# Performance work log

Hardware: AMD Instinct MI355X
Metric: run time of the kernel (lower is better)

The kernel has to match this reference:

```python
import jax, jax.numpy as jnp
import numpy as np

HIDDEN = 6      # tiny MLP width
GRID_R = 16     # CAM grid resolution
NUM_LAYERS = 2  # num hidden layers == shared_cam.num_layers
OUT_DIM = 3
N_POINTS = 2_097_152
LN_EPS = 1e-5


def _bilinear_border(grid, xy):
    """F.grid_sample(mode='bilinear', padding_mode='border', align_corners=True)
    for point queries. grid: [C, R, R]; xy: [N, 2] in [-1, 1] with xy[:,0]=x
    (width) and xy[:,1]=y (height). Returns [N, C]."""
    R = grid.shape[-1]
    # align_corners=True mapping to pixel coords, border padding = clamp
    coords = jnp.clip((xy + 1.0) * 0.5 * (R - 1), 0.0, float(R - 1))
    ix, iy = coords[:, 0], coords[:, 1]
    x0f, y0f = jnp.floor(ix), jnp.floor(iy)
    wx, wy = ix - x0f, iy - y0f                       # [N]
    x0 = x0f.astype(jnp.int32)
    y0 = y0f.astype(jnp.int32)
    x1 = jnp.minimum(x0 + 1, R - 1)
    y1 = jnp.minimum(y0 + 1, R - 1)
    g00 = grid[:, y0, x0]  # [C, N]
    g01 = grid[:, y0, x1]
    g10 = grid[:, y1, x0]
    g11 = grid[:, y1, x1]
    top = g00 * (1.0 - wx) + g01 * wx
    bot = g10 * (1.0 - wx) + g11 * wx
    return (top * (1.0 - wy) + bot * wy).T            # [N, C]


def _layernorm(h, w, b):
    mu = jnp.mean(h, axis=-1, keepdims=True)
    var = jnp.mean((h - mu) ** 2, axis=-1, keepdims=True)  # biased, like torch LN
    return (h - mu) * jax.lax.rsqrt(var + LN_EPS) * w + b


def setup_inputs() -> dict:
    key = jax.random.key(0)
    ks = jax.random.split(key, 10)
    xy = jax.random.uniform(ks[0], (N_POINTS, 2), dtype=jnp.float32,
                            minval=-1.0, maxval=1.0)
    # CAM grids (init is ones/zeros; perturb so the math is exercised)
    gamma = 1.0 + 0.1 * jax.random.normal(ks[1], (NUM_LAYERS, HIDDEN, GRID_R, GRID_R), jnp.float32)
    beta = 0.1 * jax.random.normal(ks[2], (NUM_LAYERS, HIDDEN, GRID_R, GRID_R), jnp.float32)
    # Tiny MLP weights (Kaiming-ish scale)
    w_in = jax.random.normal(ks[3], (HIDDEN, 2), jnp.float32) / np.sqrt(2.0)
    b_in = 0.1 * jax.random.normal(ks[4], (HIDDEN,), jnp.float32)
    w_h = jax.random.normal(ks[5], (NUM_LAYERS - 1, HIDDEN, HIDDEN), jnp.float32) / np.sqrt(HIDDEN)
    b_h = 0.1 * jax.random.normal(ks[6], (NUM_LAYERS - 1, HIDDEN), jnp.float32)
    w_out = jax.random.normal(ks[7], (OUT_DIM, HIDDEN), jnp.float32) / np.sqrt(HIDDEN)
    b_out = 0.1 * jax.random.normal(ks[8], (OUT_DIM,), jnp.float32)
    ln_w = 1.0 + 0.05 * jax.random.normal(ks[9], (NUM_LAYERS, HIDDEN), jnp.float32)
    ln_b = jnp.zeros((NUM_LAYERS, HIDDEN), jnp.float32)
    return {"xy": xy, "gamma": gamma, "beta": beta, "w_in": w_in, "b_in": b_in,
            "w_h": w_h, "b_h": b_h, "w_out": w_out, "b_out": b_out,
            "ln_w": ln_w, "ln_b": ln_b}


def reference(xy, gamma, beta, w_in, b_in, w_h, b_h, w_out, b_out, ln_w, ln_b):
    # h = act(in_layer(xy))
    h = jax.nn.silu(xy @ w_in.T + b_in)                    # [N, HIDDEN]
    for i in range(NUM_LAYERS):
        if i > 0:
            h = jax.nn.silu(h @ w_h[i - 1].T + b_h[i - 1])
        g = _bilinear_border(gamma[i], xy)                 # [N, HIDDEN]
        bb = _bilinear_border(beta[i], xy)                 # [N, HIDDEN]
        h = g * _layernorm(h, ln_w[i], ln_b[i]) + bb
    return h @ w_out.T + b_out                             # [N, OUT_DIM]
```

## Files before the change

### kernel.cpp

```cpp
#include <hip/hip_runtime.h>
#include <hip/hip_fp16.h>
#include <stdint.h>

#define NPTS 2097152
#define BLOCK 256
#define PPT 4
#define NBLK (NPTS / (BLOCK * PPT))

typedef float f32x2 __attribute__((ext_vector_type(2)));

static __device__ __forceinline__ float rfl(float v) {
    return __int_as_float(__builtin_amdgcn_readfirstlane(__float_as_int(v)));
}
static __device__ __forceinline__ __half2 u2h(uint32_t u) {
    union { uint32_t i; __half2 h; } v; v.i = u; return v.h;
}
static __device__ __forceinline__ uint32_t h2u(__half2 h) {
    union { __half2 h; uint32_t i; } v; v.h = h; return v.i;
}
static __device__ __forceinline__ f32x2 fma2(f32x2 a, f32x2 b, f32x2 c) {
    return __builtin_elementwise_fma(a, b, c);
}
static __device__ __forceinline__ f32x2 silu2(f32x2 v) {
    f32x2 t = v * (-1.4426950408889634f);
    f32x2 e = { __builtin_amdgcn_exp2f(t.x), __builtin_amdgcn_exp2f(t.y) };
    f32x2 d = e + 1.0f;
    f32x2 r = { __builtin_amdgcn_rcpf(d.x), __builtin_amdgcn_rcpf(d.y) };
    return v * r;
}
static __device__ __forceinline__ void ln2_apply(f32x2* h, const f32x2* g, const f32x2* b)
{
    f32x2 mu = (h[0] + h[1] + h[2] + h[3] + h[4] + h[5]) * (1.0f / 6.0f);
    f32x2 d[6];
    f32x2 var = (f32x2)0.0f;
#pragma unroll
    for (int j = 0; j < 6; ++j) { d[j] = h[j] - mu; var = fma2(d[j], d[j], var); }
    f32x2 vv = var * (1.0f / 6.0f) + 1e-5f;
    f32x2 rs = { __builtin_amdgcn_rsqf(vv.x), __builtin_amdgcn_rsqf(vv.y) };
#pragma unroll
    for (int j = 0; j < 6; ++j)
        h[j] = fma2(g[j], d[j] * rs, b[j]);
}

__global__ __launch_bounds__(256) void pack_kernel(
    const float* __restrict__ gamma,
    const float* __restrict__ beta,
    const float* __restrict__ ln_w,
    const float* __restrict__ ln_b,
    uint32_t* __restrict__ ws)
{
    int idx = blockIdx.x * 256 + threadIdx.x;
    if (idx >= 3072) return;
    int l = (idx >= 1536) ? 1 : 0;
    int r = idx - l * 1536;
    int s = r >> 8;
    int cell = r & 255;
    int x = cell & 15;
    int x1 = (x < 15) ? x + 1 : 15;
    int rowb = cell - x;
    int ch0 = (s < 3) ? 2 * s : 2 * (s - 3);
    const float* gsrc = gamma + l * 1536 + ch0 * 256;
    float ga_lo = gsrc[rowb + x];
    float ga_hi = gsrc[256 + rowb + x];
    float gb_lo = gsrc[rowb + x1];
    float gb_hi = gsrc[256 + rowb + x1];
    float a_lo, a_hi, b_lo, b_hi;
    if (s < 3) {
        float w_lo = ln_w[6 * l + ch0];
        float w_hi = ln_w[6 * l + ch0 + 1];
        a_lo = ga_lo * w_lo; a_hi = ga_hi * w_hi;
        b_lo = gb_lo * w_lo; b_hi = gb_hi * w_hi;
    } else {
        const float* bsrc = beta + l * 1536 + ch0 * 256;
        float nb_lo = ln_b[6 * l + ch0];
        float nb_hi = ln_b[6 * l + ch0 + 1];
        a_lo = fmaf(ga_lo, nb_lo, bsrc[rowb + x]);
        a_hi = fmaf(ga_hi, nb_hi, bsrc[256 + rowb + x]);
        b_lo = fmaf(gb_lo, nb_lo, bsrc[rowb + x1]);
        b_hi = fmaf(gb_hi, nb_hi, bsrc[256 + rowb + x1]);
    }
    uint32_t* dst = ws + (l * 256 + cell) * 12 + 2 * s;
    dst[0] = h2u(__floats2half2_rn(a_lo, a_hi));
    dst[1] = h2u(__floats2half2_rn(b_lo, b_hi));
}

static __device__ __forceinline__ void interp6_c(
    const uint4* u,
    __half2 W00, __half2 W01, __half2 W10, __half2 W11,
    f32x2* g, f32x2* b, int c)
{
    uint32_t A[6]  = { u[0].x, u[0].z, u[1].x, u[1].z, u[2].x, u[2].z };
    uint32_t Bv[6] = { u[0].y, u[0].w, u[1].y, u[1].w, u[2].y, u[2].w };
    uint32_t C[6]  = { u[3].x, u[3].z, u[4].x, u[4].z, u[5].x, u[5].z };
    uint32_t D[6]  = { u[3].y, u[3].w, u[4].y, u[4].w, u[5].y, u[5].w };
#pragma unroll
    for (int s = 0; s < 6; ++s) {
        __half2 acc = __hmul2(u2h(A[s]), W00);
        acc = __hfma2(u2h(Bv[s]), W01, acc);
        acc = __hfma2(u2h(C[s]), W10, acc);
        acc = __hfma2(u2h(D[s]), W11, acc);
        float2 r = __half22float2(acc);
        if (s < 3) { g[2 * s][c] = r.x; g[2 * s + 1][c] = r.y; }
        else       { b[2 * (s - 3)][c] = r.x; b[2 * (s - 3) + 1][c] = r.y; }
    }
}

__global__ __launch_bounds__(BLOCK, 4) void camfield_kernel(
    const float* __restrict__ xy,
    const uint32_t* __restrict__ packed,
    const float* __restrict__ w_in,
    const float* __restrict__ b_in,
    const float* __restrict__ w_h,
    const float* __restrict__ b_h,
    const float* __restrict__ w_out,
    const float* __restrict__ b_out,
    float* __restrict__ out)
{
    __shared__ __align__(16) uint32_t sg[2][256][12];

    const int tid = threadIdx.x;

    const int p0 = (blockIdx.x * BLOCK + tid) * PPT;
    const float4* xv = (const float4*)(xy + 2 * p0);
    float4 q0 = xv[0];
    float4 q1 = xv[1];

    {
        const uint4* src = (const uint4*)packed;
        uint4* dst = (uint4*)&sg[0][0][0];
#pragma unroll
        for (int i = 0; i < 6; ++i)
            dst[tid + 256 * i] = src[tid + 256 * i];
    }

    float Win0[6], Win1[6], Bin[6], Wh[6][6], Bh[6], Wo[3][6], Bo[3];
#pragma unroll
    for (int j = 0; j < 6; ++j) {
        Win0[j] = w_in[2 * j];
        Win1[j] = w_in[2 * j + 1];
        Bin[j]  = b_in[j];
        Bh[j]   = rfl(b_h[j]);
#pragma unroll
        for (int k = 0; k < 6; ++k) Wh[j][k] = rfl(w_h[6 * j + k]);
    }
#pragma unroll
    for (int j = 0; j < 3; ++j) {
        Bo[j] = rfl(b_out[j]);
#pragma unroll
        for (int k = 0; k < 6; ++k) Wo[j][k] = rfl(w_out[6 * j + k]);
    }

    __syncthreads();

    float xs[4] = { q0.x, q0.z, q1.x, q1.z };
    float ys[4] = { q0.y, q0.w, q1.y, q1.w };

    float o[12];

#pragma unroll
    for (int pp = 0; pp < 2; ++pp) {
        __half2 Wq[2][4];
        const uint4* c4[2];
        f32x2 X, Y;
#pragma unroll
        for (int c = 0; c < 2; ++c) {
            const int p = 2 * pp + c;
            const float x = xs[p];
            const float y = ys[p];
            X[c] = x; Y[c] = y;
            float fx = fminf(fmaxf(fmaf(x, 7.5f, 7.5f), 0.0f), 15.0f);
            float fy = fminf(fmaxf(fmaf(y, 7.5f, 7.5f), 0.0f), 15.0f);
            int x0 = (int)fx; if (x0 > 14) x0 = 14;
            int y0 = (int)fy; if (y0 > 14) y0 = 14;
            float wx = fx - (float)x0;
            float wy = fy - (float)y0;
            float w11f = wx * wy;
            float w10f = wy - w11f;
            float w01f = wx - w11f;
            float w00f = 1.0f - wx - wy + w11f;
            Wq[c][0] = __float2half2_rn(w00f);
            Wq[c][1] = __float2half2_rn(w01f);
            Wq[c][2] = __float2half2_rn(w10f);
            Wq[c][3] = __float2half2_rn(w11f);
            c4[c] = (const uint4*)&sg[0][(y0 << 4) + x0][0];
        }

        uint4 u[2][6];
#pragma unroll
        for (int c = 0; c < 2; ++c) {
            u[c][0] = c4[c][0];  u[c][1] = c4[c][1];  u[c][2] = c4[c][2];
            u[c][3] = c4[c][48]; u[c][4] = c4[c][49]; u[c][5] = c4[c][50];
        }

        f32x2 h2[6];
#pragma unroll
        for (int j = 0; j < 6; ++j)
            h2[j] = silu2(fma2(X, (f32x2)Win0[j], fma2(Y, (f32x2)Win1[j], (f32x2)Bin[j])));

        f32x2 G[6], Bb[6];
        interp6_c(u[0], Wq[0][0], Wq[0][1], Wq[0][2], Wq[0][3], G, Bb, 0);
        interp6_c(u[1], Wq[1][0], Wq[1][1], Wq[1][2], Wq[1][3], G, Bb, 1);
        ln2_apply(h2, G, Bb);

        uint4 v[2][6];
#pragma unroll
        for (int c = 0; c < 2; ++c) {
            v[c][0] = c4[c][768]; v[c][1] = c4[c][769]; v[c][2] = c4[c][770];
            v[c][3] = c4[c][816]; v[c][4] = c4[c][817]; v[c][5] = c4[c][818];
        }

        f32x2 t2[6];
#pragma unroll
        for (int j = 0; j < 6; ++j) {
            f32x2 a = (f32x2)Bh[j];
#pragma unroll
            for (int k = 0; k < 6; ++k) a = fma2(h2[k], (f32x2)Wh[j][k], a);
            t2[j] = silu2(a);
        }

        interp6_c(v[0], Wq[0][0], Wq[0][1], Wq[0][2], Wq[0][3], G, Bb, 0);
        interp6_c(v[1], Wq[1][0], Wq[1][1], Wq[1][2], Wq[1][3], G, Bb, 1);
        ln2_apply(t2, G, Bb);

#pragma unroll
        for (int j = 0; j < 3; ++j) {
            f32x2 a = (f32x2)Bo[j];
#pragma unroll
            for (int k = 0; k < 6; ++k) a = fma2(t2[k], (f32x2)Wo[j][k], a);
            o[3 * (2 * pp) + j]     = a.x;
            o[3 * (2 * pp + 1) + j] = a.y;
        }
    }

    float4* op = (float4*)(out + 3 * p0);
#pragma unroll
    for (int q = 0; q < 3; ++q)
        op[q] = make_float4(o[4 * q], o[4 * q + 1], o[4 * q + 2], o[4 * q + 3]);
}

extern "C" void kernel_launch(void* const* d_in, const int* in_sizes, int n_in,
                              void* d_out, int out_size, void* d_ws, size_t ws_size,
                              hipStream_t stream) {
    pack_kernel<<<12, 256, 0, stream>>>(
        (const float*)d_in[1],
        (const float*)d_in[2],
        (const float*)d_in[9],
        (const float*)d_in[10],
        (uint32_t*)d_ws);
    camfield_kernel<<<NBLK, BLOCK, 0, stream>>>(
        (const float*)d_in[0],
        (const uint32_t*)d_ws,
        (const float*)d_in[3],
        (const float*)d_in[4],
        (const float*)d_in[5],
        (const float*)d_in[6],
        (const float*)d_in[7],
        (const float*)d_in[8],
        (float*)d_out);
}
```

Baseline: 103.1 us.

## Interleave LDS grid gathers with LayerNorm stats and shrink register footprint

Restructures the per-pair loop so the bilinear gathers are issued row by row per point and interleaved with the LayerNorm mean/variance computation, instead of loading all twelve uint4 per point up front. This lowers live registers and overlaps LDS latency with ALU work. It also merges the two SiLU reciprocals into one shared rcp, makes w_in wave-uniform via readfirstlane, and writes outputs per iteration rather than buffering all twelve. The shared reciprocal changes rounding slightly and can overflow for large intermediate values.

```diff
diff --git a/kernel.cpp b/kernel.cpp
--- a/kernel.cpp
+++ b/kernel.cpp
@@ -25,21 +25,18 @@
     f32x2 t = v * (-1.4426950408889634f);
     f32x2 e = { __builtin_amdgcn_exp2f(t.x), __builtin_amdgcn_exp2f(t.y) };
     f32x2 d = e + 1.0f;
-    f32x2 r = { __builtin_amdgcn_rcpf(d.x), __builtin_amdgcn_rcpf(d.y) };
-    return v * r;
-}
-static __device__ __forceinline__ void ln2_apply(f32x2* h, const f32x2* g, const f32x2* b)
-{
+    float r = __builtin_amdgcn_rcpf(d.x * d.y);
+    f32x2 inv = { r * d.y, r * d.x };
+    return v * inv;
+}
+static __device__ __forceinline__ void ln2_prep(const f32x2* h, f32x2* d, f32x2* rs) {
     f32x2 mu = (h[0] + h[1] + h[2] + h[3] + h[4] + h[5]) * (1.0f / 6.0f);
-    f32x2 d[6];
     f32x2 var = (f32x2)0.0f;
 #pragma unroll
     for (int j = 0; j < 6; ++j) { d[j] = h[j] - mu; var = fma2(d[j], d[j], var); }
     f32x2 vv = var * (1.0f / 6.0f) + 1e-5f;
-    f32x2 rs = { __builtin_amdgcn_rsqf(vv.x), __builtin_amdgcn_rsqf(vv.y) };
-#pragma unroll
-    for (int j = 0; j < 6; ++j)
-        h[j] = fma2(g[j], d[j] * rs, b[j]);
+    f32x2 r = { __builtin_amdgcn_rsqf(vv.x), __builtin_amdgcn_rsqf(vv.y) };
+    *rs = r;
 }
 
 __global__ __launch_bounds__(256) void pack_kernel(
@@ -84,25 +81,48 @@
     dst[1] = h2u(__floats2half2_rn(b_lo, b_hi));
 }
 
-static __device__ __forceinline__ void interp6_c(
-    const uint4* u,
-    __half2 W00, __half2 W01, __half2 W10, __half2 W11,
-    f32x2* g, f32x2* b, int c)
-{
-    uint32_t A[6]  = { u[0].x, u[0].z, u[1].x, u[1].z, u[2].x, u[2].z };
-    uint32_t Bv[6] = { u[0].y, u[0].w, u[1].y, u[1].w, u[2].y, u[2].w };
-    uint32_t C[6]  = { u[3].x, u[3].z, u[4].x, u[4].z, u[5].x, u[5].z };
-    uint32_t D[6]  = { u[3].y, u[3].w, u[4].y, u[4].w, u[5].y, u[5].w };
+static __device__ __forceinline__ void interp_row(
+    uint4 r0, uint4 r1, uint4 r2, __half2 Wa, __half2 Wb, __half2* acc, bool first)
+{
+    uint32_t A[6] = { r0.x, r0.z, r1.x, r1.z, r2.x, r2.z };
+    uint32_t B[6] = { r0.y, r0.w, r1.y, r1.w, r2.y, r2.w };
 #pragma unroll
     for (int s = 0; s < 6; ++s) {
-        __half2 acc = __hmul2(u2h(A[s]), W00);
-        acc = __hfma2(u2h(Bv[s]), W01, acc);
-        acc = __hfma2(u2h(C[s]), W10, acc);
-        acc = __hfma2(u2h(D[s]), W11, acc);
-        float2 r = __half22float2(acc);
-        if (s < 3) { g[2 * s][c] = r.x; g[2 * s + 1][c] = r.y; }
-        else       { b[2 * (s - 3)][c] = r.x; b[2 * (s - 3) + 1][c] = r.y; }
-    }
+        __half2 t = first ? __hmul2(u2h(A[s]), Wa) : __hfma2(u2h(A[s]), Wa, acc[s]);
+        acc[s] = __hfma2(u2h(B[s]), Wb, t);
+    }
+}
+
+static __device__ __forceinline__ void interp_point(
+    const uint4* base, int off, const __half2* W, f32x2* G, f32x2* Bb, int c)
+{
+    uint4 r0 = base[off], r1 = base[off + 1], r2 = base[off + 2];
+    __half2 acc[6];
+    interp_row(r0, r1, r2, W[0], W[1], acc, true);
+    uint4 s0 = base[off + 48], s1 = base[off + 49], s2 = base[off + 50];
+    interp_row(s0, s1, s2, W[2], W[3], acc, false);
+#pragma unroll
+    for (int s = 0; s < 6; ++s) {
+        float2 r = __half22float2(acc[s]);
+        if (s < 3) { G[2 * s][c] = r.x; G[2 * s + 1][c] = r.y; }
+        else       { Bb[2 * (s - 3)][c] = r.x; Bb[2 * (s - 3) + 1][c] = r.y; }
+    }
+}
+
+static __device__ __forceinline__ void coordw(float x, float y, int* cell, __half2* W)
+{
+    float fx = fminf(fmaxf(fmaf(x, 7.5f, 7.5f), 0.0f), 15.0f);
+    float fy = fminf(fmaxf(fmaf(y, 7.5f, 7.5f), 0.0f), 15.0f);
+    int x0 = (int)fx; if (x0 > 14) x0 = 14;
+    int y0 = (int)fy; if (y0 > 14) y0 = 14;
+    float wx = fx - (float)x0;
+    float wy = fy - (float)y0;
+    float w11 = wx * wy;
+    W[0] = __float2half2_rn(1.0f - wx - wy + w11);
+    W[1] = __float2half2_rn(wx - w11);
+    W[2] = __float2half2_rn(wy - w11);
+    W[3] = __float2half2_rn(w11);
+    *cell = (y0 << 4) + x0;
 }
 
 __global__ __launch_bounds__(BLOCK, 4) void camfield_kernel(
@@ -136,8 +156,8 @@
     float Win0[6], Win1[6], Bin[6], Wh[6][6], Bh[6], Wo[3][6], Bo[3];
 #pragma unroll
     for (int j = 0; j < 6; ++j) {
-        Win0[j] = w_in[2 * j];
-        Win1[j] = w_in[2 * j + 1];
+        Win0[j] = rfl(w_in[2 * j]);
+        Win1[j] = rfl(w_in[2 * j + 1]);
         Bin[j]  = b_in[j];
         Bh[j]   = rfl(b_h[j]);
 #pragma unroll
@@ -152,45 +172,23 @@
 
     __syncthreads();
 
-    float xs[4] = { q0.x, q0.z, q1.x, q1.z };
-    float ys[4] = { q0.y, q0.w, q1.y, q1.w };
-
-    float o[12];
+    float* ob = out + 3 * p0;
 
 #pragma unroll
     for (int pp = 0; pp < 2; ++pp) {
-        __half2 Wq[2][4];
-        const uint4* c4[2];
-        f32x2 X, Y;
-#pragma unroll
-        for (int c = 0; c < 2; ++c) {
-            const int p = 2 * pp + c;
-            const float x = xs[p];
-            const float y = ys[p];
-            X[c] = x; Y[c] = y;
-            float fx = fminf(fmaxf(fmaf(x, 7.5f, 7.5f), 0.0f), 15.0f);
-            float fy = fminf(fmaxf(fmaf(y, 7.5f, 7.5f), 0.0f), 15.0f);
-            int x0 = (int)fx; if (x0 > 14) x0 = 14;
-            int y0 = (int)fy; if (y0 > 14) y0 = 14;
-            float wx = fx - (float)x0;
-            float wy = fy - (float)y0;
-            float w11f = wx * wy;
-            float w10f = wy - w11f;
-            float w01f = wx - w11f;
-            float w00f = 1.0f - wx - wy + w11f;
-            Wq[c][0] = __float2half2_rn(w00f);
-            Wq[c][1] = __float2half2_rn(w01f);
-            Wq[c][2] = __float2half2_rn(w10f);
-            Wq[c][3] = __float2half2_rn(w11f);
-            c4[c] = (const uint4*)&sg[0][(y0 << 4) + x0][0];
-        }
-
-        uint4 u[2][6];
-#pragma unroll
-        for (int c = 0; c < 2; ++c) {
-            u[c][0] = c4[c][0];  u[c][1] = c4[c][1];  u[c][2] = c4[c][2];
-            u[c][3] = c4[c][48]; u[c][4] = c4[c][49]; u[c][5] = c4[c][50];
-        }
+        const float xa = (pp == 0) ? q0.x : q1.x;
+        const float ya = (pp == 0) ? q0.y : q1.y;
+        const float xb = (pp == 0) ? q0.z : q1.z;
+        const float yb = (pp == 0) ? q0.w : q1.w;
+        const f32x2 X = { xa, xb };
+        const f32x2 Y = { ya, yb };
+
+        int cellA, cellB;
+        __half2 WA[4], WB[4];
+        coordw(xa, ya, &cellA, WA);
+        coordw(xb, yb, &cellB, WB);
+        const uint4* cA = (const uint4*)&sg[0][cellA][0];
+        const uint4* cB = (const uint4*)&sg[0][cellB][0];
 
         f32x2 h2[6];
 #pragma unroll
@@ -198,16 +196,13 @@
             h2[j] = silu2(fma2(X, (f32x2)Win0[j], fma2(Y, (f32x2)Win1[j], (f32x2)Bin[j])));
 
         f32x2 G[6], Bb[6];
-        interp6_c(u[0], Wq[0][0], Wq[0][1], Wq[0][2], Wq[0][3], G, Bb, 0);
-        interp6_c(u[1], Wq[1][0], Wq[1][1], Wq[1][2], Wq[1][3], G, Bb, 1);
-        ln2_apply(h2, G, Bb);
-
-        uint4 v[2][6];
-#pragma unroll
-        for (int c = 0; c < 2; ++c) {
-            v[c][0] = c4[c][768]; v[c][1] = c4[c][769]; v[c][2] = c4[c][770];
-            v[c][3] = c4[c][816]; v[c][4] = c4[c][817]; v[c][5] = c4[c][818];
-        }
+        interp_point(cA, 0, WA, G, Bb, 0);
+        f32x2 d[6], rs;
+        ln2_prep(h2, d, &rs);
+        interp_point(cB, 0, WB, G, Bb, 1);
+#pragma unroll
+        for (int j = 0; j < 6; ++j)
+            h2[j] = fma2(G[j], d[j] * rs, Bb[j]);
 
         f32x2 t2[6];
 #pragma unroll
@@ -217,25 +212,29 @@
             for (int k = 0; k < 6; ++k) a = fma2(h2[k], (f32x2)Wh[j][k], a);
             t2[j] = silu2(a);
         }
-
-        interp6_c(v[0], Wq[0][0], Wq[0][1], Wq[0][2], Wq[0][3], G, Bb, 0);
-        interp6_c(v[1], Wq[1][0], Wq[1][1], Wq[1][2], Wq[1][3], G, Bb, 1);
-        ln2_apply(t2, G, Bb);
-
+        interp_point(cA, 768, WA, G, Bb, 0);
+        ln2_prep(t2, d, &rs);
+        interp_point(cB, 768, WB, G, Bb, 1);
+#pragma unroll
+        for (int j = 0; j < 6; ++j)
+            t2[j] = fma2(G[j], d[j] * rs, Bb[j]);
+
+        f32x2 ov[3];
 #pragma unroll
         for (int j = 0; j < 3; ++j) {
             f32x2 a = (f32x2)Bo[j];
 #pragma unroll
             for (int k = 0; k < 6; ++k) a = fma2(t2[k], (f32x2)Wo[j][k], a);
-            o[3 * (2 * pp) + j]     = a.x;
-            o[3 * (2 * pp + 1) + j] = a.y;
+            ov[j] = a;
         }
-    }
-
-    float4* op = (float4*)(out + 3 * p0);
-#pragma unroll
-    for (int q = 0; q < 3; ++q)
-        op[q] = make_float4(o[4 * q], o[4 * q + 1], o[4 * q + 2], o[4 * q + 3]);
+        if (pp == 0) {
+            *(float4*)(ob)     = make_float4(ov[0].x, ov[1].x, ov[2].x, ov[0].y);
+            *(float2*)(ob + 4) = make_float2(ov[1].y, ov[2].y);
+        } else {
+            *(float2*)(ob + 6) = make_float2(ov[0].x, ov[1].x);
+            *(float4*)(ob + 8) = make_float4(ov[2].x, ov[0].y, ov[1].y, ov[2].y);
+        }
+    }
 }
 
 extern "C" void kernel_launch(void* const* d_in, const int* in_sizes, int n_in,
```

Result: no change. 105.0 us (+1.8%).
